# Optimization experiments

Measured on AMD Instinct MI355X. Metric: run time of the kernel, lower is better.

## Reference

```python
import jax, jax.numpy as jnp
import numpy as np

EMBED_DIM = 1024
NUM_HEADS = 16
SEQ = 2048
BATCH = 2


def setup_inputs() -> dict:
    key = jax.random.key(0)
    ks = jax.random.split(key, 9)
    E = EMBED_DIM
    gain = 1.0 / np.sqrt(2.0)  # xavier_uniform with gain 1/sqrt(2) (qkv_same_dim)
    limit = gain * np.sqrt(6.0 / (E + E))
    q = jax.random.normal(ks[0], (SEQ, BATCH, E), dtype=jnp.float32)
    k = jax.random.normal(ks[1], (SEQ, BATCH, E), dtype=jnp.float32)
    v = jax.random.normal(ks[2], (SEQ, BATCH, E), dtype=jnp.float32)
    Wq = jax.random.uniform(ks[3], (E, E), jnp.float32, -limit, limit)
    Wk = jax.random.uniform(ks[4], (E, E), jnp.float32, -limit, limit)
    Wv = jax.random.uniform(ks[5], (E, E), jnp.float32, -limit, limit)
    bq = jnp.zeros((E,), jnp.float32)
    bk = jnp.zeros((E,), jnp.float32)
    bv = jnp.zeros((E,), jnp.float32)
    return {"query": q, "key": k, "value": v,
            "Wq": Wq, "bq": bq, "Wk": Wk, "bk": bk, "Wv": Wv, "bv": bv}


def reference(query, key, value, Wq, bq, Wk, bk, Wv, bv):
    # Base Taylor attention path (norm_taylor=True, do_scale=True, has_out=False).
    L, B, E = query.shape
    H = NUM_HEADS
    hd = E // H
    scaling = E ** (-0.5)  # self.scaling = dim**-0.5, dim == embed_dim

    q = (query @ Wq + bq) * scaling          # (L, B, E)
    k = key @ Wk + bk                         # (S, B, E)
    v = value @ Wv + bv                       # (S, B, E)

    def split_heads(x):
        # (T, B, E) -> (B*H, T, hd)
        T = x.shape[0]
        return x.reshape(T, B * H, hd).transpose(1, 0, 2)

    qh, kh, vh = split_heads(q), split_heads(k), split_heads(v)

    # Taylor expansion of exp(qk) to first order: 1 + q.k
    attn = 1.0 + jnp.einsum('bld,bsd->bls', qh, kh)   # (B*H, L, S)
    attn = attn / attn.sum(axis=-1, keepdims=True)    # row-normalize
    out = jnp.einsum('bls,bsd->bld', attn, vh)        # (B*H, L, hd)
    out = out.transpose(1, 0, 2).reshape(L, B, E)     # (L, B, E)
    return out
```

## Files before the change

kernel.cpp:

```cpp
#include <hip/hip_runtime.h>
#include <hip/hip_bf16.h>

#define L_SEQ 2048
#define BATCH 2
#define ROWS 4096
#define E 1024
#define NH 16
#define HD 64

typedef __attribute__((ext_vector_type(4))) float f32x4;
typedef __attribute__((ext_vector_type(8))) __bf16 bf16x8;

#define SWZ(byt) ((byt) ^ ((((byt) >> 7) & 7) << 4))

__device__ __forceinline__ void gload16(const void* g, void* l) {
    __builtin_amdgcn_global_load_lds((const __attribute__((address_space(1))) void*)g,
                                     (__attribute__((address_space(3))) void*)l,
                                     16, 0, 0);
}

__global__ __launch_bounds__(256) void convert_x(const float* __restrict__ q,
                                                 const float* __restrict__ k,
                                                 const float* __restrict__ v,
                                                 __bf16* __restrict__ Xb) {
    const int z = blockIdx.y;
    const float* src = (z == 0) ? q : ((z == 1) ? k : v);
    __bf16* dst = Xb + (size_t)z * ROWS * E;
    const size_t i = ((size_t)blockIdx.x * 256 + threadIdx.x) * 8;
    const float4 a = *(const float4*)(src + i);
    const float4 b = *(const float4*)(src + i + 4);
    bf16x8 o;
    o[0] = (__bf16)a.x; o[1] = (__bf16)a.y; o[2] = (__bf16)a.z; o[3] = (__bf16)a.w;
    o[4] = (__bf16)b.x; o[5] = (__bf16)b.y; o[6] = (__bf16)b.z; o[7] = (__bf16)b.w;
    *(bf16x8*)(dst + i) = o;
}

__global__ __launch_bounds__(256) void transpose_w(const float* __restrict__ Wq,
                                                   const float* __restrict__ Wk,
                                                   const float* __restrict__ Wv,
                                                   __bf16* __restrict__ Wt) {
    const int z = blockIdx.z;
    const float* W = (z == 0) ? Wq : ((z == 1) ? Wk : Wv);
    __bf16* dst = Wt + (size_t)z * E * E;
    __shared__ __align__(16) float t[64][65];
    const int n0 = blockIdx.x * 64, k0 = blockIdx.y * 64;
    const int r = threadIdx.x >> 2, c4 = threadIdx.x & 3;
#pragma unroll
    for (int j = 0; j < 4; ++j) {
        const float4 vv = *(const float4*)&W[(size_t)(k0 + r) * E + n0 + c4 * 16 + j * 4];
        t[r][c4 * 16 + j * 4 + 0] = vv.x;
        t[r][c4 * 16 + j * 4 + 1] = vv.y;
        t[r][c4 * 16 + j * 4 + 2] = vv.z;
        t[r][c4 * 16 + j * 4 + 3] = vv.w;
    }
    __syncthreads();
    bf16x8 o0, o1;
#pragma unroll
    for (int j = 0; j < 8; ++j) {
        o0[j] = (__bf16)t[c4 * 16 + j][r];
        o1[j] = (__bf16)t[c4 * 16 + 8 + j][r];
    }
    *(bf16x8*)&dst[(size_t)(n0 + r) * E + k0 + c4 * 16] = o0;
    *(bf16x8*)&dst[(size_t)(n0 + r) * E + k0 + c4 * 16 + 8] = o1;
}

__global__ __launch_bounds__(256) void gemm_qkv(const __bf16* __restrict__ Xb,
                                                const __bf16* __restrict__ Wt,
                                                const float* __restrict__ bq,
                                                const float* __restrict__ bk,
                                                const float* __restrict__ bv,
                                                __bf16* __restrict__ Cb) {
    const int z = blockIdx.z;
    const __bf16* A = Xb + (size_t)z * ROWS * E;
    const __bf16* Bm = Wt + (size_t)z * E * E;
    __bf16* C = Cb + (size_t)z * ROWS * E;
    const float* bias = (z == 0) ? bq : ((z == 1) ? bk : bv);
    const float alpha = (z == 0) ? 0.03125f : 1.0f;
    const int m0 = blockIdx.y * 128, n0 = blockIdx.x * 128;
    __shared__ __align__(16) __bf16 lsA[128 * 32];
    __shared__ __align__(16) __bf16 lsB[128 * 32];
    const int tid = threadIdx.x;
    const int lane = tid & 63, wave = tid >> 6;
    const int lr = lane & 15, kg = lane >> 4;
    const int wm = (wave >> 1) * 64, wn = (wave & 1) * 64;
    f32x4 acc[4][4] = {};
    for (int kt = 0; kt < E; kt += 32) {
        __syncthreads();
#pragma unroll
        for (int i = 0; i < 2; ++i) {
            const int idx = i * 256 + tid;
            const int row = idx >> 2, c8 = (idx & 3) * 8;
            gload16(A + (size_t)(m0 + row) * E + kt + c8, &lsA[(i * 256 + wave * 64) * 8]);
            gload16(Bm + (size_t)(n0 + row) * E + kt + c8, &lsB[(i * 256 + wave * 64) * 8]);
        }
        __syncthreads();
        bf16x8 af[4], bfr[4];
#pragma unroll
        for (int mi = 0; mi < 4; ++mi)
            af[mi] = *(const bf16x8*)&lsA[(wm + mi * 16 + lr) * 32 + kg * 8];
#pragma unroll
        for (int ni = 0; ni < 4; ++ni)
            bfr[ni] = *(const bf16x8*)&lsB[(wn + ni * 16 + lr) * 32 + kg * 8];
#pragma unroll
        for (int mi = 0; mi < 4; ++mi)
#pragma unroll
            for (int ni = 0; ni < 4; ++ni)
                acc[mi][ni] = __builtin_amdgcn_mfma_f32_16x16x32_bf16(af[mi], bfr[ni], acc[mi][ni], 0, 0, 0);
    }
#pragma unroll
    for (int mi = 0; mi < 4; ++mi)
#pragma unroll
        for (int ni = 0; ni < 4; ++ni) {
            const int col = n0 + wn + ni * 16 + lr;
            const int rbase = m0 + wm + mi * 16 + kg * 4;
            const float bcol = bias[col];
#pragma unroll
            for (int rr = 0; rr < 4; ++rr)
                C[(size_t)(rbase + rr) * E + col] = (__bf16)((acc[mi][ni][rr] + bcol) * alpha);
        }
}

__global__ __launch_bounds__(256) void reduce_kv(const __bf16* __restrict__ Kb,
                                                 const __bf16* __restrict__ Vb,
                                                 float* __restrict__ Mpart,
                                                 float* __restrict__ ksumP,
                                                 float* __restrict__ vsumP) {
    const int bh = blockIdx.x, b = bh >> 4, h = bh & 15;
    const int ts = blockIdx.y;
    const int t0 = ts * 128;
    __shared__ __align__(16) __bf16 sK[128 * 64];
    __shared__ __align__(16) __bf16 sV[128 * 64];
    __shared__ float red_k[4][64];
    __shared__ float red_v[4][64];
    const int tid = threadIdx.x;
    const int lane = tid & 63, wave = tid >> 6;
    const int lr = lane & 15, kg = lane >> 4;

    float vk[8] = {}, vv[8] = {};
    const int d0 = (tid & 7) * 8;
#pragma unroll
    for (int i = 0; i < 4; ++i) {
        const int t = i * 32 + (tid >> 3);
        const size_t g = (size_t)((t0 + t) * 2 + b) * E + h * 64 + d0;
        const bf16x8 kv = *(const bf16x8*)&Kb[g];
        const bf16x8 vvv = *(const bf16x8*)&Vb[g];
        const int lo = (t * 128 + d0 * 2) ^ (wave << 5);
        *(bf16x8*)((char*)sK + lo) = kv;
        *(bf16x8*)((char*)sV + lo) = vvv;
#pragma unroll
        for (int j = 0; j < 8; ++j) { vk[j] += (float)kv[j]; vv[j] += (float)vvv[j]; }
    }
#pragma unroll
    for (int m = 8; m <= 32; m <<= 1)
#pragma unroll
        for (int j = 0; j < 8; ++j) {
            vk[j] += __shfl_xor(vk[j], m, 64);
            vv[j] += __shfl_xor(vv[j], m, 64);
        }
    if (lane < 8)
#pragma unroll
        for (int j = 0; j < 8; ++j) {
            red_k[wave][lane * 8 + j] = vk[j];
            red_v[wave][lane * 8 + j] = vv[j];
        }
    __syncthreads();

    f32x4 acc[4] = {};
#pragma unroll
    for (int kt = 0; kt < 4; ++kt) {
        const int tb = kt * 32;
        bf16x8 afr, bfr[4];
        const char* pv = (const char*)sV + (((tb + kg * 8) * 128 + (wave * 16 + lr) * 2) ^ (kg << 5));
#pragma unroll
        for (int j = 0; j < 8; ++j) afr[j] = *(const __bf16*)(pv + j * 128);
#pragma unroll
        for (int ni = 0; ni < 4; ++ni) {
            const char* pk = (const char*)sK + (((tb + kg * 8) * 128 + (ni * 16 + lr) * 2) ^ (kg << 5));
#pragma unroll
            for (int j = 0; j < 8; ++j) bfr[ni][j] = *(const __bf16*)(pk + j * 128);
        }
#pragma unroll
        for (int ni = 0; ni < 4; ++ni)
            acc[ni] = __builtin_amdgcn_mfma_f32_16x16x32_bf16(afr, bfr[ni], acc[ni], 0, 0, 0);
    }

    float* Mp = Mpart + ((size_t)bh * 16 + ts) * 4096;
#pragma unroll
    for (int ni = 0; ni < 4; ++ni)
#pragma unroll
        for (int rr = 0; rr < 4; ++rr)
            Mp[(wave * 16 + kg * 4 + rr) * 64 + ni * 16 + lr] = acc[ni][rr];
    if (tid < 64)
        ksumP[(bh * 16 + ts) * 64 + tid] = red_k[0][tid] + red_k[1][tid] + red_k[2][tid] + red_k[3][tid];
    else if (tid < 128) {
        const int d = tid - 64;
        vsumP[(bh * 16 + ts) * 64 + d] = red_v[0][d] + red_v[1][d] + red_v[2][d] + red_v[3][d];
    }
}

__global__ __launch_bounds__(256) void combine_m(const float* __restrict__ Mpart,
                                                 const float* __restrict__ ksumP,
                                                 const float* __restrict__ vsumP,
                                                 float* __restrict__ Mt,
                                                 float* __restrict__ ksum,
                                                 float* __restrict__ vsum) {
    const int blk = blockIdx.x, tid = threadIdx.x;
    if (blk < 256) {
        const int e2 = (blk * 256 + tid) * 2;
        const int bh = e2 >> 12, r = e2 & 4095;
        const float* src = Mpart + (size_t)bh * 16 * 4096 + r;
        float s0 = 0.f, s1 = 0.f;
#pragma unroll
        for (int ts = 0; ts < 16; ++ts) {
            s0 += src[ts * 4096];
            s1 += src[ts * 4096 + 1];
        }
        Mt[(size_t)bh * 4096 + r] = s0;
        Mt[(size_t)bh * 4096 + r + 1] = s1;
    } else if (blk < 264) {
        const int idx = (blk - 256) * 256 + tid;
        const int bh = idx >> 6, d = idx & 63;
        float s = 0.f;
#pragma unroll
        for (int ts = 0; ts < 16; ++ts) s += ksumP[bh * 1024 + ts * 64 + d];
        ksum[idx] = s;
    } else {
        const int idx = (blk - 264) * 256 + tid;
        const int bh = idx >> 6, d = idx & 63;
        float s = 0.f;
#pragma unroll
        for (int ts = 0; ts < 16; ++ts) s += vsumP[bh * 1024 + ts * 64 + d];
        vsum[idx] = s;
    }
}

__global__ __launch_bounds__(256) void taylor_out(const __bf16* __restrict__ Qb,
                                                  const float* __restrict__ Mt,
                                                  const float* __restrict__ ksum,
                                                  const float* __restrict__ vsum,
                                                  float* __restrict__ out) {
    const int b = blockIdx.y;
    const int lblk = blockIdx.x * 16;
    const int tid = threadIdx.x, lane = tid & 63, wave = tid >> 6;
    const int lr = lane & 15, kg = lane >> 4;
    __shared__ __align__(16) __bf16 sM[4][4096];
    for (int hh = 0; hh < 4; ++hh) {
        __syncthreads();
#pragma unroll
        for (int i = 0; i < 8; ++i) {
            const int idx = i * 256 + tid;
            const int hseg = idx >> 9, rem = idx & 511;
            const float* src = &Mt[(size_t)(b * 16 + hseg * 4 + hh) * 4096 + rem * 8];
            const float4 mA = *(const float4*)src;
            const float4 mB = *(const float4*)(src + 4);
            bf16x8 o;
            o[0] = (__bf16)mA.x; o[1] = (__bf16)mA.y; o[2] = (__bf16)mA.z; o[3] = (__bf16)mA.w;
            o[4] = (__bf16)mB.x; o[5] = (__bf16)mB.y; o[6] = (__bf16)mB.z; o[7] = (__bf16)mB.w;
            *(bf16x8*)((char*)&sM[hseg][0] + SWZ(rem * 16)) = o;
        }
        __syncthreads();
        const int h = wave * 4 + hh;
        const int bh = b * 16 + h;
        const int rA = (lblk + lr) * 2 + b;
        const bf16x8 a0 = *(const bf16x8*)&Qb[(size_t)rA * E + h * 64 + kg * 8];
        const bf16x8 a1 = *(const bf16x8*)&Qb[(size_t)rA * E + h * 64 + 32 + kg * 8];
        float p = 0.f;
        const float* ks = &ksum[bh * 64];
#pragma unroll
        for (int j = 0; j < 8; ++j)
            p += (float)a0[j] * ks[kg * 8 + j] + (float)a1[j] * ks[32 + kg * 8 + j];
        p += __shfl_xor(p, 16, 64);
        p += __shfl_xor(p, 32, 64);
        const float Z = 2048.0f + p;
        f32x4 acc[4] = {};
#pragma unroll
        for (int ni = 0; ni < 4; ++ni) {
            const int byt0 = (ni * 16 + lr) * 128 + kg * 16;
            const bf16x8 b0 = *(const bf16x8*)((const char*)&sM[wave][0] + SWZ(byt0));
            const bf16x8 b1 = *(const bf16x8*)((const char*)&sM[wave][0] + SWZ(byt0 + 64));
            acc[ni] = __builtin_amdgcn_mfma_f32_16x16x32_bf16(a0, b0, acc[ni], 0, 0, 0);
            acc[ni] = __builtin_amdgcn_mfma_f32_16x16x32_bf16(a1, b1, acc[ni], 0, 0, 0);
        }
        float invZ[4];
#pragma unroll
        for (int rr = 0; rr < 4; ++rr) invZ[rr] = 1.0f / __shfl(Z, kg * 4 + rr, 64);
        const float* vs = &vsum[bh * 64];
#pragma unroll
        for (int ni = 0; ni < 4; ++ni)
#pragma unroll
            for (int rr = 0; rr < 4; ++rr) {
                const int l_out = lblk + kg * 4 + rr;
                out[(size_t)(l_out * 2 + b) * E + h * 64 + ni * 16 + lr] =
                    (vs[ni * 16 + lr] + acc[ni][rr]) * invZ[rr];
            }
    }
}

extern "C" void kernel_launch(void* const* d_in, const int* in_sizes, int n_in,
                              void* d_out, int out_size, void* d_ws, size_t ws_size,
                              hipStream_t stream) {
    const float* q  = (const float*)d_in[0];
    const float* k  = (const float*)d_in[1];
    const float* v  = (const float*)d_in[2];
    const float* Wq = (const float*)d_in[3];
    const float* bq = (const float*)d_in[4];
    const float* Wk = (const float*)d_in[5];
    const float* bk = (const float*)d_in[6];
    const float* Wv = (const float*)d_in[7];
    const float* bv = (const float*)d_in[8];
    float* out = (float*)d_out;
    char* w = (char*)d_ws;
    __bf16* Xb = (__bf16*)(w);
    __bf16* Wt = (__bf16*)(w + 25165824);
    __bf16* Cb = (__bf16*)(w + 31457280);
    float* Mt   = (float*)(w + 56623104);
    float* ksum = (float*)(w + 57147392);
    float* vsum = (float*)(w + 57155584);
    float* Mpart = (float*)(w);
    float* ksumP = (float*)(w + 8388608);
    float* vsumP = (float*)(w + 8519680);

    convert_x<<<dim3(2048, 3), 256, 0, stream>>>(q, k, v, Xb);
    transpose_w<<<dim3(16, 16, 3), 256, 0, stream>>>(Wq, Wk, Wv, Wt);
    gemm_qkv<<<dim3(8, 32, 3), 256, 0, stream>>>(Xb, Wt, bq, bk, bv, Cb);
    reduce_kv<<<dim3(32, 16), 256, 0, stream>>>(Cb + (size_t)ROWS * E,
                                                Cb + 2 * (size_t)ROWS * E, Mpart, ksumP, vsumP);
    combine_m<<<272, 256, 0, stream>>>(Mpart, ksumP, vsumP, Mt, ksum, vsum);
    taylor_out<<<dim3(128, 2), 256, 0, stream>>>(Cb, Mt, ksum, vsum, out);
}
```

Baseline: 83.77 us.

## Rewrite QKV GEMM as 256x256 tiled, double-buffered pipelined MFMA kernel

Replaces the 128x128, single-buffered QKV projection GEMM with a 256x256 tile kernel using 512 threads, 128KB of dynamic LDS double buffering, and an XOR-swizzled LDS layout. Global-to-LDS loads for the next K slice are issued between MFMA phases, and barriers plus s_setprio interleave compute with the loads. The goal is to hide memory latency, cut LDS bank conflicts and raise per-block data reuse. The cost is a much larger LDS footprint and only 192 blocks for the device. The hand-written vmcnt waits and barriers also add correctness risk.

```diff
diff --git a/kernel.cpp b/kernel.cpp
--- a/kernel.cpp
+++ b/kernel.cpp
@@ -64,60 +64,112 @@
     *(bf16x8*)&dst[(size_t)(n0 + r) * E + k0 + c4 * 16 + 8] = o1;
 }
 
-__global__ __launch_bounds__(256) void gemm_qkv(const __bf16* __restrict__ Xb,
-                                                const __bf16* __restrict__ Wt,
-                                                const float* __restrict__ bq,
-                                                const float* __restrict__ bk,
-                                                const float* __restrict__ bv,
-                                                __bf16* __restrict__ Cb) {
+__device__ __forceinline__ void stage_ht(const __bf16* __restrict__ gsrc, int row0, int kcol,
+                                         char* ldsdst, int wv, int ln) {
+#pragma unroll
+    for (int r = 0; r < 2; ++r) {
+        const int rowg = row0 + r * 64 + wv * 8 + (ln >> 3);
+        const int c16 = (ln & 7) ^ (ln >> 3);
+        gload16(gsrc + (size_t)rowg * E + kcol + c16 * 8,
+                ldsdst + r * 8192 + wv * 1024);
+    }
+}
+
+__device__ __forceinline__ bf16x8 fragld(const char* base, int row, int kk, int kg) {
+    return *(const bf16x8*)(base + row * 128 + ((((kk << 2) | kg) ^ (row & 7)) << 4));
+}
+
+#define PH_SYNC_BEGIN  __builtin_amdgcn_s_barrier(); \
+                       asm volatile("s_waitcnt lgkmcnt(0)" ::: "memory"); \
+                       __builtin_amdgcn_sched_barrier(0); \
+                       __builtin_amdgcn_s_setprio(1);
+#define PH_SYNC_END    __builtin_amdgcn_s_setprio(0); \
+                       __builtin_amdgcn_s_barrier();
+
+__global__ __launch_bounds__(512, 2) void gemm_qkv(const __bf16* __restrict__ Xb,
+                                                   const __bf16* __restrict__ Wt,
+                                                   const float* __restrict__ bq,
+                                                   const float* __restrict__ bk,
+                                                   const float* __restrict__ bv,
+                                                   __bf16* __restrict__ Cb) {
+    extern __shared__ __align__(16) char smem[];
     const int z = blockIdx.z;
     const __bf16* A = Xb + (size_t)z * ROWS * E;
-    const __bf16* Bm = Wt + (size_t)z * E * E;
+    const __bf16* B = Wt + (size_t)z * E * E;
     __bf16* C = Cb + (size_t)z * ROWS * E;
     const float* bias = (z == 0) ? bq : ((z == 1) ? bk : bv);
     const float alpha = (z == 0) ? 0.03125f : 1.0f;
-    const int m0 = blockIdx.y * 128, n0 = blockIdx.x * 128;
-    __shared__ __align__(16) __bf16 lsA[128 * 32];
-    __shared__ __align__(16) __bf16 lsB[128 * 32];
-    const int tid = threadIdx.x;
-    const int lane = tid & 63, wave = tid >> 6;
-    const int lr = lane & 15, kg = lane >> 4;
-    const int wm = (wave >> 1) * 64, wn = (wave & 1) * 64;
-    f32x4 acc[4][4] = {};
-    for (int kt = 0; kt < E; kt += 32) {
-        __syncthreads();
-#pragma unroll
-        for (int i = 0; i < 2; ++i) {
-            const int idx = i * 256 + tid;
-            const int row = idx >> 2, c8 = (idx & 3) * 8;
-            gload16(A + (size_t)(m0 + row) * E + kt + c8, &lsA[(i * 256 + wave * 64) * 8]);
-            gload16(Bm + (size_t)(n0 + row) * E + kt + c8, &lsB[(i * 256 + wave * 64) * 8]);
-        }
-        __syncthreads();
-        bf16x8 af[4], bfr[4];
-#pragma unroll
-        for (int mi = 0; mi < 4; ++mi)
-            af[mi] = *(const bf16x8*)&lsA[(wm + mi * 16 + lr) * 32 + kg * 8];
-#pragma unroll
-        for (int ni = 0; ni < 4; ++ni)
-            bfr[ni] = *(const bf16x8*)&lsB[(wn + ni * 16 + lr) * 32 + kg * 8];
-#pragma unroll
-        for (int mi = 0; mi < 4; ++mi)
-#pragma unroll
-            for (int ni = 0; ni < 4; ++ni)
-                acc[mi][ni] = __builtin_amdgcn_mfma_f32_16x16x32_bf16(af[mi], bfr[ni], acc[mi][ni], 0, 0, 0);
-    }
-#pragma unroll
-    for (int mi = 0; mi < 4; ++mi)
-#pragma unroll
-        for (int ni = 0; ni < 4; ++ni) {
-            const int col = n0 + wn + ni * 16 + lr;
-            const int rbase = m0 + wm + mi * 16 + kg * 4;
+    const int m0 = blockIdx.y * 256, n0 = blockIdx.x * 256;
+    const int tid = threadIdx.x, ln = tid & 63, wv = tid >> 6;
+    const int lr = ln & 15, kg = ln >> 4;
+    const int wm = (wv & 3) * 64, wn = (wv >> 2) * 128;
+    char* LA0 = smem;            char* LA1 = smem + 32768;
+    char* LB0 = smem + 65536;    char* LB1 = smem + 98304;
+
+    stage_ht(A, m0 + 0,   0,  LA0 + 0,     wv, ln);
+    stage_ht(A, m0 + 128, 0,  LA0 + 16384, wv, ln);
+    stage_ht(B, n0 + 0,   0,  LB0 + 0,     wv, ln);
+    stage_ht(B, n0 + 128, 0,  LB0 + 16384, wv, ln);
+    stage_ht(A, m0 + 0,   64, LA1 + 0,     wv, ln);
+    stage_ht(A, m0 + 128, 64, LA1 + 16384, wv, ln);
+    asm volatile("s_waitcnt vmcnt(4)" ::: "memory");
+    __builtin_amdgcn_s_barrier();
+
+    f32x4 acc[4][8] = {};
+    bf16x8 Af[4][2], Bf[2][2];
+
+#define LOAD_B(nb) \
+    _Pragma("unroll") for (int nn = 0; nn < 2; ++nn) \
+    _Pragma("unroll") for (int kk = 0; kk < 2; ++kk) \
+        Bf[nn][kk] = fragld(cB, wn + ((nb) + nn) * 16 + lr, kk, kg);
+#define QUAD(q) \
+    _Pragma("unroll") for (int m = 0; m < 4; ++m) \
+    _Pragma("unroll") for (int nn = 0; nn < 2; ++nn) \
+    _Pragma("unroll") for (int kk = 0; kk < 2; ++kk) \
+        acc[m][2 * (q) + nn] = __builtin_amdgcn_mfma_f32_16x16x32_bf16(Af[m][kk], Bf[nn][kk], acc[m][2 * (q) + nn], 0, 0, 0);
+
+    for (int T = 0; T < 16; ++T) {
+        const char* cA = (T & 1) ? LA1 : LA0;
+        const char* cB = (T & 1) ? LB1 : LB0;
+        char* nB = (T & 1) ? LB0 : LB1;
+        char* nA = (T & 1) ? LA1 : LA0;
+#pragma unroll
+        for (int m = 0; m < 4; ++m)
+#pragma unroll
+            for (int kk = 0; kk < 2; ++kk)
+                Af[m][kk] = fragld(cA, wm + m * 16 + lr, kk, kg);
+        LOAD_B(0);
+        if (T < 15) stage_ht(B, n0 + 0, (T + 1) * 64, nB + 0, wv, ln);
+        PH_SYNC_BEGIN; QUAD(0); PH_SYNC_END;
+        LOAD_B(2);
+        if (T < 15) stage_ht(B, n0 + 128, (T + 1) * 64, nB + 16384, wv, ln);
+        PH_SYNC_BEGIN; QUAD(1); PH_SYNC_END;
+        LOAD_B(4);
+        if (T < 14) stage_ht(A, m0 + 0, (T + 2) * 64, nA + 0, wv, ln);
+        PH_SYNC_BEGIN; QUAD(2); PH_SYNC_END;
+        LOAD_B(6);
+        if (T < 14) stage_ht(A, m0 + 128, (T + 2) * 64, nA + 16384, wv, ln);
+        PH_SYNC_BEGIN; QUAD(3);
+        __builtin_amdgcn_s_setprio(0);
+        if (T < 14)       { asm volatile("s_waitcnt vmcnt(4)" ::: "memory"); }
+        else if (T == 14) { asm volatile("s_waitcnt vmcnt(0)" ::: "memory"); }
+        __builtin_amdgcn_s_barrier();
+    }
+#undef LOAD_B
+#undef QUAD
+
+#pragma unroll
+    for (int m = 0; m < 4; ++m) {
+        const int rbase = m0 + wm + m * 16 + kg * 4;
+#pragma unroll
+        for (int n = 0; n < 8; ++n) {
+            const int col = n0 + wn + n * 16 + lr;
             const float bcol = bias[col];
 #pragma unroll
             for (int rr = 0; rr < 4; ++rr)
-                C[(size_t)(rbase + rr) * E + col] = (__bf16)((acc[mi][ni][rr] + bcol) * alpha);
-        }
+                C[(size_t)(rbase + rr) * E + col] = (__bf16)((acc[m][n][rr] + bcol) * alpha);
+        }
+    }
 }
 
 __global__ __launch_bounds__(256) void reduce_kv(const __bf16* __restrict__ Kb,
@@ -320,9 +372,11 @@
     float* ksumP = (float*)(w + 8388608);
     float* vsumP = (float*)(w + 8519680);
 
+    hipFuncSetAttribute((const void*)gemm_qkv,
+                        hipFuncAttributeMaxDynamicSharedMemorySize, 131072);
     convert_x<<<dim3(2048, 3), 256, 0, stream>>>(q, k, v, Xb);
     transpose_w<<<dim3(16, 16, 3), 256, 0, stream>>>(Wq, Wk, Wv, Wt);
-    gemm_qkv<<<dim3(8, 32, 3), 256, 0, stream>>>(Xb, Wt, bq, bk, bv, Cb);
+    gemm_qkv<<<dim3(4, 16, 3), 512, 131072, stream>>>(Xb, Wt, bq, bk, bv, Cb);
     reduce_kv<<<dim3(32, 16), 256, 0, stream>>>(Cb + (size_t)ROWS * E,
                                                 Cb + 2 * (size_t)ROWS * E, Mpart, ksumP, vsumP);
     combine_m<<<272, 256, 0, stream>>>(Mpart, ksumP, vsumP, Mt, ksum, vsum);
```

Result: faster. 77.44 us (-7.6%).

## Merge prep kernels, swizzle GEMM LDS layout, and reorder GEMM grid

Applied to the files above, without the earlier changes.

Fuses the activation bf16 conversion and the weight transpose into one launch so that a kernel launch and its tail drain are removed. In the QKV GEMM, the global source column is XOR-swizzled per lane so that the data lands in LDS in swizzled order, and fragment reads apply the matching XOR to avoid LDS bank conflicts. The grid mapping is also swapped so that consecutive blocks walk along M rather than N, which changes L2 reuse of the weight tiles. The swizzle must match exactly between the load and the read, or the results will be wrong.

```diff
diff --git a/kernel.cpp b/kernel.cpp
--- a/kernel.cpp
+++ b/kernel.cpp
@@ -19,31 +19,32 @@
                                      16, 0, 0);
 }
 
-__global__ __launch_bounds__(256) void convert_x(const float* __restrict__ q,
-                                                 const float* __restrict__ k,
-                                                 const float* __restrict__ v,
-                                                 __bf16* __restrict__ Xb) {
+__global__ __launch_bounds__(256) void prep(const float* __restrict__ q,
+                                            const float* __restrict__ k,
+                                            const float* __restrict__ v,
+                                            const float* __restrict__ Wq,
+                                            const float* __restrict__ Wk,
+                                            const float* __restrict__ Wv,
+                                            __bf16* __restrict__ Xb,
+                                            __bf16* __restrict__ Wt) {
     const int z = blockIdx.y;
-    const float* src = (z == 0) ? q : ((z == 1) ? k : v);
-    __bf16* dst = Xb + (size_t)z * ROWS * E;
-    const size_t i = ((size_t)blockIdx.x * 256 + threadIdx.x) * 8;
-    const float4 a = *(const float4*)(src + i);
-    const float4 b = *(const float4*)(src + i + 4);
-    bf16x8 o;
-    o[0] = (__bf16)a.x; o[1] = (__bf16)a.y; o[2] = (__bf16)a.z; o[3] = (__bf16)a.w;
-    o[4] = (__bf16)b.x; o[5] = (__bf16)b.y; o[6] = (__bf16)b.z; o[7] = (__bf16)b.w;
-    *(bf16x8*)(dst + i) = o;
-}
-
-__global__ __launch_bounds__(256) void transpose_w(const float* __restrict__ Wq,
-                                                   const float* __restrict__ Wk,
-                                                   const float* __restrict__ Wv,
-                                                   __bf16* __restrict__ Wt) {
-    const int z = blockIdx.z;
+    if (blockIdx.x < 2048) {
+        const float* src = (z == 0) ? q : ((z == 1) ? k : v);
+        __bf16* dst = Xb + (size_t)z * ROWS * E;
+        const size_t i = ((size_t)blockIdx.x * 256 + threadIdx.x) * 8;
+        const float4 a = *(const float4*)(src + i);
+        const float4 b = *(const float4*)(src + i + 4);
+        bf16x8 o;
+        o[0] = (__bf16)a.x; o[1] = (__bf16)a.y; o[2] = (__bf16)a.z; o[3] = (__bf16)a.w;
+        o[4] = (__bf16)b.x; o[5] = (__bf16)b.y; o[6] = (__bf16)b.z; o[7] = (__bf16)b.w;
+        *(bf16x8*)(dst + i) = o;
+        return;
+    }
     const float* W = (z == 0) ? Wq : ((z == 1) ? Wk : Wv);
     __bf16* dst = Wt + (size_t)z * E * E;
     __shared__ __align__(16) float t[64][65];
-    const int n0 = blockIdx.x * 64, k0 = blockIdx.y * 64;
+    const int tt = blockIdx.x - 2048;
+    const int n0 = (tt & 15) * 64, k0 = (tt >> 4) * 64;
     const int r = threadIdx.x >> 2, c4 = threadIdx.x & 3;
 #pragma unroll
     for (int j = 0; j < 4; ++j) {
@@ -62,6 +63,10 @@
     }
     *(bf16x8*)&dst[(size_t)(n0 + r) * E + k0 + c4 * 16] = o0;
     *(bf16x8*)&dst[(size_t)(n0 + r) * E + k0 + c4 * 16 + 8] = o1;
+}
+
+__device__ __forceinline__ bf16x8 fragld32(const char* base, int row, int kg) {
+    return *(const bf16x8*)(base + row * 64 + ((kg ^ (row & 3)) << 4));
 }
 
 __global__ __launch_bounds__(256) void gemm_qkv(const __bf16* __restrict__ Xb,
@@ -76,31 +81,32 @@
     __bf16* C = Cb + (size_t)z * ROWS * E;
     const float* bias = (z == 0) ? bq : ((z == 1) ? bk : bv);
     const float alpha = (z == 0) ? 0.03125f : 1.0f;
-    const int m0 = blockIdx.y * 128, n0 = blockIdx.x * 128;
+    const int m0 = blockIdx.x * 128, n0 = blockIdx.y * 128;
     __shared__ __align__(16) __bf16 lsA[128 * 32];
     __shared__ __align__(16) __bf16 lsB[128 * 32];
     const int tid = threadIdx.x;
-    const int lane = tid & 63, wave = tid >> 6;
-    const int lr = lane & 15, kg = lane >> 4;
-    const int wm = (wave >> 1) * 64, wn = (wave & 1) * 64;
+    const int ln = tid & 63, wv = tid >> 6;
+    const int lr = ln & 15, kg = ln >> 4;
+    const int wm = (wv >> 1) * 64, wn = (wv & 1) * 64;
+    const int cs = (((ln & 3) ^ ((ln >> 2) & 3)) << 3);
     f32x4 acc[4][4] = {};
     for (int kt = 0; kt < E; kt += 32) {
         __syncthreads();
 #pragma unroll
         for (int i = 0; i < 2; ++i) {
             const int idx = i * 256 + tid;
-            const int row = idx >> 2, c8 = (idx & 3) * 8;
-            gload16(A + (size_t)(m0 + row) * E + kt + c8, &lsA[(i * 256 + wave * 64) * 8]);
-            gload16(Bm + (size_t)(n0 + row) * E + kt + c8, &lsB[(i * 256 + wave * 64) * 8]);
+            const int row = idx >> 2;
+            gload16(A + (size_t)(m0 + row) * E + kt + cs, &lsA[(i * 256 + wv * 64) * 8]);
+            gload16(Bm + (size_t)(n0 + row) * E + kt + cs, &lsB[(i * 256 + wv * 64) * 8]);
         }
         __syncthreads();
         bf16x8 af[4], bfr[4];
 #pragma unroll
         for (int mi = 0; mi < 4; ++mi)
-            af[mi] = *(const bf16x8*)&lsA[(wm + mi * 16 + lr) * 32 + kg * 8];
+            af[mi] = fragld32((const char*)lsA, wm + mi * 16 + lr, kg);
 #pragma unroll
         for (int ni = 0; ni < 4; ++ni)
-            bfr[ni] = *(const bf16x8*)&lsB[(wn + ni * 16 + lr) * 32 + kg * 8];
+            bfr[ni] = fragld32((const char*)lsB, wn + ni * 16 + lr, kg);
 #pragma unroll
         for (int mi = 0; mi < 4; ++mi)
 #pragma unroll
@@ -320,9 +326,8 @@
     float* ksumP = (float*)(w + 8388608);
     float* vsumP = (float*)(w + 8519680);
 
-    convert_x<<<dim3(2048, 3), 256, 0, stream>>>(q, k, v, Xb);
-    transpose_w<<<dim3(16, 16, 3), 256, 0, stream>>>(Wq, Wk, Wv, Wt);
-    gemm_qkv<<<dim3(8, 32, 3), 256, 0, stream>>>(Xb, Wt, bq, bk, bv, Cb);
+    prep<<<dim3(2304, 3), 256, 0, stream>>>(q, k, v, Wq, Wk, Wv, Xb, Wt);
+    gemm_qkv<<<dim3(32, 8, 3), 256, 0, stream>>>(Xb, Wt, bq, bk, bv, Cb);
     reduce_kv<<<dim3(32, 16), 256, 0, stream>>>(Cb + (size_t)ROWS * E,
                                                 Cb + 2 * (size_t)ROWS * E, Mpart, ksumP, vsumP);
     combine_m<<<272, 256, 0, stream>>>(Mpart, ksumP, vsumP, Mt, ksum, vsum);
```

Measured after the change: 77.94 us. -7.0%, faster.
